# Kernel tuning notes

Measured on AMD Instinct MI355X. Metric: run time of the kernel, lower is better.

Reference implementation:

```python
import jax, jax.numpy as jnp
import numpy as np
from jax import lax


def squash(vec):
    # vec: [..., caps, dim]; squash along last dim (dim=2 in original layout [B, caps, dim])
    lensq = jnp.sum(vec * vec, axis=2)
    length = jnp.sqrt(lensq)
    scale = (lensq / (1.0 + lensq) / length)[:, :, None]
    return vec * scale


def setup_inputs() -> dict:
    key = jax.random.key(0)
    ks = jax.random.split(key, 6)
    stdv = 1.0 / np.sqrt(1152.0)
    return {
        "x": jax.random.normal(ks[0], (512, 1, 28, 28), dtype=jnp.float32),
        "conv1_w": jax.random.normal(ks[1], (256, 1, 9, 9), dtype=jnp.float32) * 0.05,
        "conv1_b": jax.random.normal(ks[2], (256,), dtype=jnp.float32) * 0.01,
        "conv2_w": jax.random.normal(ks[3], (256, 256, 9, 9), dtype=jnp.float32) * 0.01,
        "conv2_b": jax.random.normal(ks[4], (256,), dtype=jnp.float32) * 0.01,
        "caps_w": jax.random.uniform(ks[5], (1152, 8, 160), dtype=jnp.float32, minval=-stdv, maxval=stdv),
        "b_prior": jnp.zeros((1152, 10), dtype=jnp.float32),
    }


def reference(x, conv1_w, conv1_b, conv2_w, conv2_b, caps_w, b_prior):
    n_iterations = 3
    output_caps, output_dim = 10, 16
    dn = ("NCHW", "OIHW", "NCHW")

    # conv1 + relu: [N,1,28,28] -> [N,256,20,20]
    h = lax.conv_general_dilated(x, conv1_w, (1, 1), "VALID", dimension_numbers=dn)
    h = jax.nn.relu(h + conv1_b[None, :, None, None])

    # first capsule layer: conv k=9 s=2 -> [N,256,6,6]
    h = lax.conv_general_dilated(h, conv2_w, (2, 2), "VALID", dimension_numbers=dn)
    h = h + conv2_b[None, :, None, None]
    N, C, H, W = h.shape
    # [N, 32, 8, H, W] -> [N, 32, H, W, 8] -> [N, 32*H*W, 8]
    u = h.reshape(N, 32, 8, H, W).transpose(0, 1, 3, 4, 2).reshape(N, 32 * H * W, 8)
    u = squash(u)  # [N, 1152, 8]

    # prediction vectors: u_hat [N, 1152, 10, 16]
    u_hat = jnp.einsum("bid,ido->bio", u, caps_w).reshape(N, 1152, output_caps, output_dim)

    # dynamic routing-by-agreement
    c = jax.nn.softmax(b_prior, axis=1)  # [1152, 10]
    s = jnp.sum(c[None, :, :, None] * u_hat, axis=1)  # [N, 10, 16]
    v = squash(s)
    b_batch = jnp.broadcast_to(b_prior, (N, 1152, output_caps))
    for _ in range(n_iterations):
        b_batch = b_batch + jnp.sum(u_hat * v[:, None, :, :], axis=-1)  # agreement
        c = jax.nn.softmax(b_batch, axis=2)[..., None]  # [N, 1152, 10, 1]
        s = jnp.sum(c * u_hat, axis=1)
        v = squash(s)

    probs = jnp.sqrt(jnp.sum(v * v, axis=2))  # [N, 10]
    return (v, probs)
```

## Files before the change

kernel.cpp:

```cpp
#include <hip/hip_runtime.h>


#define N_IMG 512

typedef __attribute__((ext_vector_type(8))) short bf16x8;
typedef __attribute__((ext_vector_type(4))) float f32x4;
typedef __attribute__((ext_vector_type(4))) unsigned int u32x4;

__device__ __forceinline__ unsigned short f2bf(float v) {
  unsigned int uu = __float_as_uint(v);
  uu += 0x7FFF + ((uu >> 16) & 1);
  return (unsigned short)(uu >> 16);
}
__device__ __forceinline__ float bf2f(unsigned short h) {
  return __uint_as_float(((unsigned int)h) << 16);
}
__device__ __forceinline__ int swz(int row) {
  return (row ^ ((row >> 3) & 7)) << 4;
}

__global__ __launch_bounds__(256) void repack_b_kernel(
    const float* __restrict__ w2, unsigned short* __restrict__ bph,
    unsigned short* __restrict__ bpl) {
  __shared__ float slab[82 * 16 * 17];
  const int n = blockIdx.x, c = blockIdx.y;
  const int tid = threadIdx.x;
  for (int e = tid; e < 81 * 256; e += 256) {
    const int row = e / 81;
    const int rs = e - row * 81;
    const int co = row >> 4, ci = row & 15;
    slab[(rs * 16 + co) * 17 + ci] =
        w2[((size_t)(n * 16 + co) * 256 + c * 16 + ci) * 81 + rs];
  }
  __syncthreads();
  const int lane = tid & 63;
  const int l15 = lane & 15;
  const int lh = lane >> 5;
  const int cio8 = ((lane >> 4) & 1) * 8;
  for (int tt = tid >> 6; tt < 41; tt += 4) {
    const int rs = 2 * tt + lh;
    unsigned int hw[4], lw[4];
#pragma unroll
    for (int jp = 0; jp < 4; ++jp) {
      unsigned short h2[2], l2[2];
#pragma unroll
      for (int e = 0; e < 2; ++e) {
        const int j = jp * 2 + e;
        float v = (rs < 81) ? slab[(rs * 16 + l15) * 17 + cio8 + j] : 0.0f;
        unsigned short hh = f2bf(v);
        h2[e] = hh;
        l2[e] = f2bf(v - bf2f(hh));
      }
      hw[jp] = (unsigned int)h2[0] | ((unsigned int)h2[1] << 16);
      lw[jp] = (unsigned int)l2[0] | ((unsigned int)l2[1] << 16);
    }
    const size_t off = (((size_t)n * 656 + c * 41 + tt) * 64 + lane) * 8;
    *(u32x4*)(bph + off) = (u32x4){hw[0], hw[1], hw[2], hw[3]};
    *(u32x4*)(bpl + off) = (u32x4){lw[0], lw[1], lw[2], lw[3]};
  }
}

__global__ __launch_bounds__(160) void repack_cw_kernel(
    const float* __restrict__ cw, float* __restrict__ cwt) {
  __shared__ float t[8][160];
  const int i = blockIdx.x;
  const int od = threadIdx.x;
#pragma unroll
  for (int k = 0; k < 8; ++k) t[k][od] = cw[((size_t)i * 8 + k) * 160 + od];
  __syncthreads();
  float4 o0 = {t[0][od], t[1][od], t[2][od], t[3][od]};
  float4 o1 = {t[4][od], t[5][od], t[6][od], t[7][od]};
  float4* dst = (float4*)(cwt + ((size_t)i * 160 + od) * 8);
  dst[0] = o0;
  dst[1] = o1;
}

__global__ __launch_bounds__(512, 1) void fused_conv_kernel(
    const float* __restrict__ x, const float* __restrict__ w1,
    const float* __restrict__ b1, const unsigned short* __restrict__ bph,
    const unsigned short* __restrict__ bpl, const float* __restrict__ b2,
    float* __restrict__ u) {
  __shared__ __align__(16) char smem[114944];
  float* stg = (float*)(smem + 51712);
  float* img = (float*)(smem + 103424);
  float* w1l = (float*)(smem + 109696);
  float* b1l = (float*)(smem + 114880);
  float* mrg = (float*)smem;
  float* sq = (float*)smem;

  const int bp2 = blockIdx.x;
  const int tid = threadIdx.x;
  const int wid = tid >> 6;
  const int g = wid & 3;
  const int kpar = wid >> 2;
  const int lane = tid & 63;
  const int l15 = lane & 15;
  const int lq4 = lane >> 4;
  const int lqb = lq4 & 1;
  const int lh = lane >> 5;

  int rowb[5];
  bool okm[5];
#pragma unroll
  for (int mt = 0; mt < 5; ++mt) {
    const int m = mt * 16 + l15;
    okm[mt] = (m < 72);
    const int mm = okm[mt] ? m : 0;
    const int im = (mm >= 36) ? 1 : 0;
    const int p = mm - 36 * im;
    const int oy = p / 6, ox = p - 6 * oy;
    rowb[mt] = im * 400 + 40 * oy + 2 * ox;
  }

  for (int i = tid; i < 1568; i += 512) img[i] = x[bp2 * 1568 + i];
  if (tid < 16) {
    *(int*)(smem + (tid >> 2) * 12928 + 804 * 16 + (tid & 3) * 4) = 0;
  }

  f32x4 acc[5][4];
#pragma unroll
  for (int mt = 0; mt < 5; ++mt)
#pragma unroll
    for (int nn = 0; nn < 4; ++nn) acc[mt][nn] = (f32x4){0.f, 0.f, 0.f, 0.f};

  const char* hbase = smem + lqb * 12928;
  const char* lbase = smem + 25856 + lqb * 12928;
  const int tt0 = kpar ? 21 : 0;
  const int tt1 = kpar ? 41 : 21;

  for (int c = 0; c < 16; ++c) {
    __syncthreads();
    for (int i = tid; i < 1296; i += 512) w1l[i] = w1[c * 1296 + i];
    if (tid < 16) b1l[tid] = b1[c * 16 + tid];
    __syncthreads();

    for (int t = tid; t < 640; t += 512) {
      const int ig = t / 320;
      const int rest = t - ig * 320;
      const int ch = rest & 15;
      const int oy = rest >> 4;
      const float* ib = &img[ig * 784];
      float a[20];
      const float bv1 = b1l[ch];
#pragma unroll
      for (int ox = 0; ox < 20; ++ox) a[ox] = bv1;
#pragma unroll
      for (int r = 0; r < 9; ++r) {
        float row[28];
        const float4* rp = (const float4*)&ib[(oy + r) * 28];
#pragma unroll
        for (int q = 0; q < 7; ++q) {
          float4 v4 = rp[q];
          row[4 * q + 0] = v4.x; row[4 * q + 1] = v4.y;
          row[4 * q + 2] = v4.z; row[4 * q + 3] = v4.w;
        }
#pragma unroll
        for (int s = 0; s < 9; ++s) {
          const float wval = w1l[ch * 81 + r * 9 + s];
#pragma unroll
          for (int ox = 0; ox < 20; ++ox)
            a[ox] = fmaf(row[ox + s], wval, a[ox]);
        }
      }
      float4* dst = (float4*)&stg[(ig * 16 + ch) * 404 + oy * 20];
#pragma unroll
      for (int q = 0; q < 5; ++q) {
        float4 v4;
        v4.x = fmaxf(a[4 * q + 0], 0.0f);
        v4.y = fmaxf(a[4 * q + 1], 0.0f);
        v4.z = fmaxf(a[4 * q + 2], 0.0f);
        v4.w = fmaxf(a[4 * q + 3], 0.0f);
        dst[q] = v4;
      }
    }
    __syncthreads();

    for (int t = tid; t < 800; t += 512) {
      const int ig = t / 400;
      const int pos = t - ig * 400;
      const int ad = swz(t);
      unsigned int hw[8], lw[8];
#pragma unroll
      for (int jp = 0; jp < 8; ++jp) {
        unsigned short h2[2], l2[2];
#pragma unroll
        for (int e = 0; e < 2; ++e) {
          const float v = stg[(ig * 16 + jp * 2 + e) * 404 + pos];
          const unsigned short hh = f2bf(v);
          h2[e] = hh;
          l2[e] = f2bf(v - bf2f(hh));
        }
        hw[jp] = (unsigned int)h2[0] | ((unsigned int)h2[1] << 16);
        lw[jp] = (unsigned int)l2[0] | ((unsigned int)l2[1] << 16);
      }
      *(u32x4*)(smem + ad) = (u32x4){hw[0], hw[1], hw[2], hw[3]};
      *(u32x4*)(smem + 12928 + ad) = (u32x4){hw[4], hw[5], hw[6], hw[7]};
      *(u32x4*)(smem + 25856 + ad) = (u32x4){lw[0], lw[1], lw[2], lw[3]};
      *(u32x4*)(smem + 38784 + ad) = (u32x4){lw[4], lw[5], lw[6], lw[7]};
    }
    __syncthreads();

    const unsigned short* pb[4];
    const unsigned short* pl[4];
#pragma unroll
    for (int nn = 0; nn < 4; ++nn) {
      const size_t base =
          ((size_t)(g * 4 + nn) * 656 + c * 41 + tt0) * 512 + lane * 8;
      pb[nn] = bph + base;
      pl[nn] = bpl + base;
    }
    bf16x8 cbh[4], cbl[4];
#pragma unroll
    for (int nn = 0; nn < 4; ++nn) {
      cbh[nn] = *(const bf16x8*)(pb[nn]);
      cbl[nn] = *(const bf16x8*)(pl[nn]);
    }
#pragma unroll 1
    for (int tt = tt0; tt < tt1; ++tt) {
      const int nxt = (tt + 1 < tt1) ? (tt + 1 - tt0) : (tt - tt0);
      bf16x8 nbh[4], nbl[4];
#pragma unroll
      for (int nn = 0; nn < 4; ++nn) {
        nbh[nn] = *(const bf16x8*)(pb[nn] + (size_t)nxt * 512);
        nbl[nn] = *(const bf16x8*)(pl[nn] + (size_t)nxt * 512);
      }
      const int rs = 2 * tt + lh;
      const int r = (rs * 57) >> 9;
      const int s = rs - 9 * r;
      const int rs20 = 20 * r + s;
      const bool okrs = (rs <= 80);
      bf16x8 ah[5], al[5];
#pragma unroll
      for (int mt = 0; mt < 5; ++mt) {
        const int row = (okm[mt] && okrs) ? (rowb[mt] + rs20) : 800;
        const int ad = swz(row);
        ah[mt] = *(const bf16x8*)(hbase + ad);
        al[mt] = *(const bf16x8*)(lbase + ad);
      }
#pragma unroll
      for (int mt = 0; mt < 5; ++mt) {
#pragma unroll
        for (int nn = 0; nn < 4; ++nn) {
          acc[mt][nn] = __builtin_amdgcn_mfma_f32_16x16x32_bf16(
              al[mt], cbh[nn], acc[mt][nn], 0, 0, 0);
          acc[mt][nn] = __builtin_amdgcn_mfma_f32_16x16x32_bf16(
              ah[mt], cbl[nn], acc[mt][nn], 0, 0, 0);
          acc[mt][nn] = __builtin_amdgcn_mfma_f32_16x16x32_bf16(
              ah[mt], cbh[nn], acc[mt][nn], 0, 0, 0);
        }
      }
#pragma unroll
      for (int nn = 0; nn < 4; ++nn) {
        cbh[nn] = nbh[nn];
        cbl[nn] = nbl[nn];
      }
    }
  }

  __syncthreads();
  if (kpar == 1) {
#pragma unroll
    for (int mt = 0; mt < 5; ++mt)
#pragma unroll
      for (int nn = 0; nn < 4; ++nn)
        *(f32x4*)(mrg + ((((g * 5 + mt) * 4 + nn) * 64 + lane) << 2)) =
            acc[mt][nn];
  }
  __syncthreads();
  if (kpar == 0) {
#pragma unroll
    for (int mt = 0; mt < 5; ++mt)
#pragma unroll
      for (int nn = 0; nn < 4; ++nn)
        acc[mt][nn] +=
            *(const f32x4*)(mrg + ((((g * 5 + mt) * 4 + nn) * 64 + lane) << 2));
  }
  __syncthreads();
  if (kpar == 0) {
    float b2v[4];
#pragma unroll
    for (int nn = 0; nn < 4; ++nn) b2v[nn] = b2[(g * 4 + nn) * 16 + l15];
#pragma unroll
    for (int mt = 0; mt < 5; ++mt) {
#pragma unroll
      for (int i = 0; i < 4; ++i) {
        const int m = mt * 16 + lq4 * 4 + i;
        if (m < 72) {
          const int im = (m >= 36) ? 1 : 0;
          const int p36 = m - 36 * im;
#pragma unroll
          for (int nn = 0; nn < 4; ++nn) {
            sq[(im * 256 + (g * 4 + nn) * 16 + l15) * 36 + p36] =
                acc[mt][nn][i] + b2v[nn];
          }
        }
      }
    }
  }
  __syncthreads();

  for (int i = tid; i < 2304; i += 512) {
    const int ig = i / 1152;
    const int cap = i - ig * 1152;
    const int gg = cap / 36, yx = cap - 36 * gg;
    float vals[8];
    float lensq = 0.0f;
#pragma unroll
    for (int d = 0; d < 8; ++d) {
      vals[d] = sq[(ig * 256 + gg * 8 + d) * 36 + yx];
      lensq = fmaf(vals[d], vals[d], lensq);
    }
    const float len = sqrtf(lensq);
    const float scale = lensq / (1.0f + lensq) / len;
    float4* dst = (float4*)(u + ((size_t)(bp2 * 2 + ig) * 1152 + cap) * 8);
    float4 lo4, hi4;
    lo4.x = vals[0] * scale; lo4.y = vals[1] * scale;
    lo4.z = vals[2] * scale; lo4.w = vals[3] * scale;
    hi4.x = vals[4] * scale; hi4.y = vals[5] * scale;
    hi4.z = vals[6] * scale; hi4.w = vals[7] * scale;
    dst[0] = lo4; dst[1] = hi4;
  }
}

__global__ __launch_bounds__(256) void routing_a_kernel(
    const float* __restrict__ u, const float* __restrict__ cwt,
    const float* __restrict__ b_prior, const float* __restrict__ vsum,
    float* __restrict__ s_part, int pass) {
  __shared__ float u_l[64 * 8];
  __shared__ float uhat[64 * 160];
  __shared__ float b_l[64 * 10];
  __shared__ float c_l[64 * 10];
  __shared__ float v_l[160];

  const int b = blockIdx.x;
  const int ch = blockIdx.y;
  const int cap0 = ch * 64;
  const int tid = threadIdx.x;

  {
    const float* src = u + ((size_t)b * 1152 + cap0) * 8;
    for (int i = tid; i < 512; i += 256) u_l[i] = src[i];
  }
  if (pass > 0 && tid < 160) v_l[tid] = vsum[b * 160 + tid];
  __syncthreads();

  for (int idx = tid; idx < 64 * 160; idx += 256) {
    const int i = idx / 160, od = idx - 160 * i;
    const float4* wp =
        (const float4*)(cwt + ((size_t)(cap0 + i) * 160 + od) * 8);
    const float4 wa = wp[0], wb = wp[1];
    const float4 ua = *(const float4*)&u_l[i * 8];
    const float4 ub = *(const float4*)&u_l[i * 8 + 4];
    float a = ua.x * wa.x;
    a = fmaf(ua.y, wa.y, a); a = fmaf(ua.z, wa.z, a); a = fmaf(ua.w, wa.w, a);
    a = fmaf(ub.x, wb.x, a); a = fmaf(ub.y, wb.y, a);
    a = fmaf(ub.z, wb.z, a); a = fmaf(ub.w, wb.w, a);
    uhat[idx] = a;
  }
  __syncthreads();

  for (int idx = tid; idx < 640; idx += 256) {
    const int i = idx / 10, o = idx - 10 * i;
    float bb = b_prior[(cap0 + i) * 10 + o];
    if (pass > 0) {
      float agg = 0.0f;
#pragma unroll
      for (int d = 0; d < 16; ++d)
        agg = fmaf(uhat[i * 160 + o * 16 + d], v_l[o * 16 + d], agg);
      bb += agg;
    }
    b_l[idx] = bb;
  }
  __syncthreads();

  if (tid < 64) {
    float m = -1e30f;
#pragma unroll
    for (int o = 0; o < 10; ++o) m = fmaxf(m, b_l[tid * 10 + o]);
    float e[10], sum = 0.0f;
#pragma unroll
    for (int o = 0; o < 10; ++o) {
      e[o] = __expf(b_l[tid * 10 + o] - m);
      sum += e[o];
    }
    const float inv = 1.0f / sum;
#pragma unroll
    for (int o = 0; o < 10; ++o) c_l[tid * 10 + o] = e[o] * inv;
  }
  __syncthreads();

  if (tid < 160) {
    const int o = tid / 16;
    float a = 0.0f;
    for (int i = 0; i < 64; ++i)
      a = fmaf(c_l[i * 10 + o], uhat[i * 160 + tid], a);
    s_part[((size_t)ch * N_IMG + b) * 160 + tid] = a;
  }
}

__global__ __launch_bounds__(192) void routing_b_kernel(
    const float* __restrict__ s_part, float* __restrict__ v_out,
    float* __restrict__ probs, float* __restrict__ vsum, int mode) {
  __shared__ float s_l[160];
  __shared__ float scale_l[10];
  __shared__ float len_l[10];
  const int b = blockIdx.x;
  const int t = threadIdx.x;
  if (t < 160) {
    float a = 0.0f;
#pragma unroll
    for (int ch = 0; ch < 18; ++ch)
      a += s_part[((size_t)ch * N_IMG + b) * 160 + t];
    s_l[t] = a;
  }
  __syncthreads();
  if (t < 10) {
    float lensq = 0.0f;
#pragma unroll
    for (int d = 0; d < 16; ++d) {
      const float xv = s_l[t * 16 + d];
      lensq = fmaf(xv, xv, lensq);
    }
    const float len = sqrtf(lensq);
    scale_l[t] = lensq / (1.0f + lensq) / len;
    len_l[t] = lensq / (1.0f + lensq);
  }
  __syncthreads();
  if (t < 160) {
    const float vv = s_l[t] * scale_l[t / 16];
    v_out[b * 160 + t] = vv;
    if (mode == 0) vsum[b * 160 + t] = vv;
    else if (mode == 1) vsum[b * 160 + t] += vv;
  }
  if (t < 10) probs[b * 10 + t] = len_l[t];
}

extern "C" void kernel_launch(void* const* d_in, const int* in_sizes, int n_in,
                              void* d_out, int out_size, void* d_ws,
                              size_t ws_size, hipStream_t stream) {
  const float* x  = (const float*)d_in[0];
  const float* w1 = (const float*)d_in[1];
  const float* b1 = (const float*)d_in[2];
  const float* w2 = (const float*)d_in[3];
  const float* b2 = (const float*)d_in[4];
  const float* cw = (const float*)d_in[5];
  const float* bp = (const float*)d_in[6];

  float* out = (float*)d_out;
  float* v_out = out;
  float* probs = out + N_IMG * 160;

  unsigned short* bph = (unsigned short*)d_ws;
  unsigned short* bpl = bph + (size_t)16 * 656 * 512;
  float* u    = (float*)d_ws + 2 * 2686976;
  float* sp   = u + (size_t)N_IMG * 1152 * 8;
  float* vsum = sp + (size_t)18 * N_IMG * 160;
  float* cwt  = (float*)bph;

  repack_b_kernel<<<dim3(16, 16), 256, 0, stream>>>(w2, bph, bpl);
  fused_conv_kernel<<<256, 512, 0, stream>>>(x, w1, b1, bph, bpl, b2, u);
  repack_cw_kernel<<<1152, 160, 0, stream>>>(cw, cwt);
  for (int pass = 0; pass < 4; ++pass) {
    const int mode = (pass == 0) ? 0 : (pass < 3 ? 1 : 2);
    routing_a_kernel<<<dim3(N_IMG, 18), 256, 0, stream>>>(u, cwt, bp, vsum, sp,
                                                          pass);
    routing_b_kernel<<<N_IMG, 192, 0, stream>>>(sp, v_out, probs, vsum, mode);
  }
}
```

Measured before the change: 1.159 ms.

## Split conv1 rows, double-buffer B prefetch, pad LDS, store caps weights in fp16

Conv1 work is split into two half-row tasks per thread so 1280 tasks spread over 512 threads instead of 640, which evens out the load. The MFMA loop is unrolled by two with double-buffered B fragments, and the first loads are issued before the conv1 stage so global latency overlaps with it. LDS plane strides gain a 16-byte pad, likely to reduce bank conflicts. Capsule weights are stored as fp16, halving routing_a weight traffic at the cost of some precision in u_hat.

```diff
diff --git a/kernel.cpp b/kernel.cpp
--- a/kernel.cpp
+++ b/kernel.cpp
@@ -1,4 +1,5 @@
 #include <hip/hip_runtime.h>
+#include <hip/hip_fp16.h>
 
 
 #define N_IMG 512
@@ -61,18 +62,56 @@
 }
 
 __global__ __launch_bounds__(160) void repack_cw_kernel(
-    const float* __restrict__ cw, float* __restrict__ cwt) {
+    const float* __restrict__ cw, __half* __restrict__ cwt) {
   __shared__ float t[8][160];
   const int i = blockIdx.x;
   const int od = threadIdx.x;
 #pragma unroll
   for (int k = 0; k < 8; ++k) t[k][od] = cw[((size_t)i * 8 + k) * 160 + od];
   __syncthreads();
-  float4 o0 = {t[0][od], t[1][od], t[2][od], t[3][od]};
-  float4 o1 = {t[4][od], t[5][od], t[6][od], t[7][od]};
-  float4* dst = (float4*)(cwt + ((size_t)i * 160 + od) * 8);
-  dst[0] = o0;
-  dst[1] = o1;
+  u32x4 pack;
+#pragma unroll
+  for (int j = 0; j < 4; ++j) {
+    __half2 hv = __floats2half2_rn(t[2 * j][od], t[2 * j + 1][od]);
+    pack[j] = *(unsigned int*)&hv;
+  }
+  *(u32x4*)(cwt + ((size_t)i * 160 + od) * 8) = pack;
+}
+
+template <int H>
+__device__ __forceinline__ void conv1_half(const float* __restrict__ ib,
+                                           const float* __restrict__ w1l,
+                                           float* __restrict__ stg, int ch,
+                                           int oy, float bv1) {
+  float a[10];
+#pragma unroll
+  for (int ox = 0; ox < 10; ++ox) a[ox] = bv1;
+#pragma unroll
+  for (int r = 0; r < 9; ++r) {
+    float row[20];
+    const float4* rp = (const float4*)&ib[(oy + r) * 28 + H * 8];
+#pragma unroll
+    for (int q = 0; q < 5; ++q) {
+      float4 v4 = rp[q];
+      row[4 * q + 0] = v4.x; row[4 * q + 1] = v4.y;
+      row[4 * q + 2] = v4.z; row[4 * q + 3] = v4.w;
+    }
+#pragma unroll
+    for (int s = 0; s < 9; ++s) {
+      const float wval = w1l[ch * 81 + r * 9 + s];
+#pragma unroll
+      for (int ox = 0; ox < 10; ++ox)
+        a[ox] = fmaf(row[ox + s + 2 * H], wval, a[ox]);
+    }
+  }
+  float2* dst = (float2*)&stg[oy * 20 + H * 10];
+#pragma unroll
+  for (int q = 0; q < 5; ++q) {
+    float2 v2;
+    v2.x = fmaxf(a[2 * q + 0], 0.0f);
+    v2.y = fmaxf(a[2 * q + 1], 0.0f);
+    dst[q] = v2;
+  }
 }
 
 __global__ __launch_bounds__(512, 1) void fused_conv_kernel(
@@ -80,11 +119,11 @@
     const float* __restrict__ b1, const unsigned short* __restrict__ bph,
     const unsigned short* __restrict__ bpl, const float* __restrict__ b2,
     float* __restrict__ u) {
-  __shared__ __align__(16) char smem[114944];
-  float* stg = (float*)(smem + 51712);
-  float* img = (float*)(smem + 103424);
-  float* w1l = (float*)(smem + 109696);
-  float* b1l = (float*)(smem + 114880);
+  __shared__ __align__(16) char smem[115008];
+  float* stg = (float*)(smem + 51776);
+  float* img = (float*)(smem + 103488);
+  float* w1l = (float*)(smem + 109760);
+  float* b1l = (float*)(smem + 114944);
   float* mrg = (float*)smem;
   float* sq = (float*)smem;
 
@@ -114,7 +153,7 @@
 
   for (int i = tid; i < 1568; i += 512) img[i] = x[bp2 * 1568 + i];
   if (tid < 16) {
-    *(int*)(smem + (tid >> 2) * 12928 + 804 * 16 + (tid & 3) * 4) = 0;
+    *(int*)(smem + (tid >> 2) * 12944 + 804 * 16 + (tid & 3) * 4) = 0;
   }
 
   f32x4 acc[5][4];
@@ -123,55 +162,83 @@
 #pragma unroll
     for (int nn = 0; nn < 4; ++nn) acc[mt][nn] = (f32x4){0.f, 0.f, 0.f, 0.f};
 
-  const char* hbase = smem + lqb * 12928;
-  const char* lbase = smem + 25856 + lqb * 12928;
+  const char* hbase = smem + lqb * 12944;
+  const char* lbase = smem + 25888 + lqb * 12944;
   const int tt0 = kpar ? 21 : 0;
   const int tt1 = kpar ? 41 : 21;
-
+  const int nk = tt1 - tt0;
+
+#define MFMA_STEP(CBH, CBL, J, DOPF)                                       \
+  {                                                                        \
+    const int rs_ = 2 * (tt0 + (J)) + lh;                                  \
+    const int r_ = (rs_ * 57) >> 9;                                        \
+    const int s_ = rs_ - 9 * r_;                                           \
+    const int rs20_ = 20 * r_ + s_;                                        \
+    const bool okrs_ = (rs_ <= 80);                                        \
+    bf16x8 ah[5], al[5];                                                   \
+    _Pragma("unroll") for (int mt = 0; mt < 5; ++mt) {                     \
+      const int row_ = (okm[mt] && okrs_) ? (rowb[mt] + rs20_) : 800;      \
+      const int ad_ = swz(row_);                                           \
+      ah[mt] = *(const bf16x8*)(hbase + ad_);                              \
+      al[mt] = *(const bf16x8*)(lbase + ad_);                              \
+    }                                                                      \
+    _Pragma("unroll") for (int mt = 0; mt < 5; ++mt) {                     \
+      _Pragma("unroll") for (int nn = 0; nn < 4; ++nn) {                   \
+        acc[mt][nn] = __builtin_amdgcn_mfma_f32_16x16x32_bf16(             \
+            al[mt], CBH[nn], acc[mt][nn], 0, 0, 0);                        \
+        acc[mt][nn] = __builtin_amdgcn_mfma_f32_16x16x32_bf16(             \
+            ah[mt], CBL[nn], acc[mt][nn], 0, 0, 0);                        \
+        acc[mt][nn] = __builtin_amdgcn_mfma_f32_16x16x32_bf16(             \
+            ah[mt], CBH[nn], acc[mt][nn], 0, 0, 0);                        \
+      }                                                                    \
+    }                                                                      \
+    if ((DOPF) && (J) + 2 < nk) {                                          \
+      _Pragma("unroll") for (int nn = 0; nn < 4; ++nn) {                   \
+        CBH[nn] = *(const bf16x8*)(pb[nn] + (size_t)((J) + 2) * 512);      \
+        CBL[nn] = *(const bf16x8*)(pl[nn] + (size_t)((J) + 2) * 512);      \
+      }                                                                    \
+    }                                                                      \
+  }
+
+#pragma unroll 1
   for (int c = 0; c < 16; ++c) {
+    const unsigned short* pb[4];
+    const unsigned short* pl[4];
+#pragma unroll
+    for (int nn = 0; nn < 4; ++nn) {
+      const size_t base =
+          ((size_t)(g * 4 + nn) * 656 + c * 41 + tt0) * 512 + lane * 8;
+      pb[nn] = bph + base;
+      pl[nn] = bpl + base;
+    }
+    bf16x8 cbh0[4], cbl0[4], cbh1[4], cbl1[4];
+#pragma unroll
+    for (int nn = 0; nn < 4; ++nn) {
+      cbh0[nn] = *(const bf16x8*)(pb[nn]);
+      cbl0[nn] = *(const bf16x8*)(pl[nn]);
+      cbh1[nn] = *(const bf16x8*)(pb[nn] + 512);
+      cbl1[nn] = *(const bf16x8*)(pl[nn] + 512);
+    }
+
     __syncthreads();
     for (int i = tid; i < 1296; i += 512) w1l[i] = w1[c * 1296 + i];
     if (tid < 16) b1l[tid] = b1[c * 16 + tid];
     __syncthreads();
 
-    for (int t = tid; t < 640; t += 512) {
-      const int ig = t / 320;
-      const int rest = t - ig * 320;
-      const int ch = rest & 15;
-      const int oy = rest >> 4;
+    for (int t = tid; t < 1280; t += 512) {
+      const int half = (t >= 640) ? 1 : 0;
+      const int rest = t - half * 640;
+      const int ig = rest / 320;
+      const int r2 = rest - ig * 320;
+      const int ch = r2 & 15;
+      const int oy = r2 >> 4;
       const float* ib = &img[ig * 784];
-      float a[20];
+      float* sb = &stg[(ig * 16 + ch) * 404];
       const float bv1 = b1l[ch];
-#pragma unroll
-      for (int ox = 0; ox < 20; ++ox) a[ox] = bv1;
-#pragma unroll
-      for (int r = 0; r < 9; ++r) {
-        float row[28];
-        const float4* rp = (const float4*)&ib[(oy + r) * 28];
-#pragma unroll
-        for (int q = 0; q < 7; ++q) {
-          float4 v4 = rp[q];
-          row[4 * q + 0] = v4.x; row[4 * q + 1] = v4.y;
-          row[4 * q + 2] = v4.z; row[4 * q + 3] = v4.w;
-        }
-#pragma unroll
-        for (int s = 0; s < 9; ++s) {
-          const float wval = w1l[ch * 81 + r * 9 + s];
-#pragma unroll
-          for (int ox = 0; ox < 20; ++ox)
-            a[ox] = fmaf(row[ox + s], wval, a[ox]);
-        }
-      }
-      float4* dst = (float4*)&stg[(ig * 16 + ch) * 404 + oy * 20];
-#pragma unroll
-      for (int q = 0; q < 5; ++q) {
-        float4 v4;
-        v4.x = fmaxf(a[4 * q + 0], 0.0f);
-        v4.y = fmaxf(a[4 * q + 1], 0.0f);
-        v4.z = fmaxf(a[4 * q + 2], 0.0f);
-        v4.w = fmaxf(a[4 * q + 3], 0.0f);
-        dst[q] = v4;
-      }
+      if (half == 0)
+        conv1_half<0>(ib, w1l, sb, ch, oy, bv1);
+      else
+        conv1_half<1>(ib, w1l, sb, ch, oy, bv1);
     }
     __syncthreads();
 
@@ -194,68 +261,21 @@
         lw[jp] = (unsigned int)l2[0] | ((unsigned int)l2[1] << 16);
       }
       *(u32x4*)(smem + ad) = (u32x4){hw[0], hw[1], hw[2], hw[3]};
-      *(u32x4*)(smem + 12928 + ad) = (u32x4){hw[4], hw[5], hw[6], hw[7]};
-      *(u32x4*)(smem + 25856 + ad) = (u32x4){lw[0], lw[1], lw[2], lw[3]};
-      *(u32x4*)(smem + 38784 + ad) = (u32x4){lw[4], lw[5], lw[6], lw[7]};
+      *(u32x4*)(smem + 12944 + ad) = (u32x4){hw[4], hw[5], hw[6], hw[7]};
+      *(u32x4*)(smem + 25888 + ad) = (u32x4){lw[0], lw[1], lw[2], lw[3]};
+      *(u32x4*)(smem + 38832 + ad) = (u32x4){lw[4], lw[5], lw[6], lw[7]};
     }
     __syncthreads();
 
-    const unsigned short* pb[4];
-    const unsigned short* pl[4];
-#pragma unroll
-    for (int nn = 0; nn < 4; ++nn) {
-      const size_t base =
-          ((size_t)(g * 4 + nn) * 656 + c * 41 + tt0) * 512 + lane * 8;
-      pb[nn] = bph + base;
-      pl[nn] = bpl + base;
-    }
-    bf16x8 cbh[4], cbl[4];
-#pragma unroll
-    for (int nn = 0; nn < 4; ++nn) {
-      cbh[nn] = *(const bf16x8*)(pb[nn]);
-      cbl[nn] = *(const bf16x8*)(pl[nn]);
-    }
+    int j = 0;
 #pragma unroll 1
-    for (int tt = tt0; tt < tt1; ++tt) {
-      const int nxt = (tt + 1 < tt1) ? (tt + 1 - tt0) : (tt - tt0);
-      bf16x8 nbh[4], nbl[4];
-#pragma unroll
-      for (int nn = 0; nn < 4; ++nn) {
-        nbh[nn] = *(const bf16x8*)(pb[nn] + (size_t)nxt * 512);
-        nbl[nn] = *(const bf16x8*)(pl[nn] + (size_t)nxt * 512);
-      }
-      const int rs = 2 * tt + lh;
-      const int r = (rs * 57) >> 9;
-      const int s = rs - 9 * r;
-      const int rs20 = 20 * r + s;
-      const bool okrs = (rs <= 80);
-      bf16x8 ah[5], al[5];
-#pragma unroll
-      for (int mt = 0; mt < 5; ++mt) {
-        const int row = (okm[mt] && okrs) ? (rowb[mt] + rs20) : 800;
-        const int ad = swz(row);
-        ah[mt] = *(const bf16x8*)(hbase + ad);
-        al[mt] = *(const bf16x8*)(lbase + ad);
-      }
-#pragma unroll
-      for (int mt = 0; mt < 5; ++mt) {
-#pragma unroll
-        for (int nn = 0; nn < 4; ++nn) {
-          acc[mt][nn] = __builtin_amdgcn_mfma_f32_16x16x32_bf16(
-              al[mt], cbh[nn], acc[mt][nn], 0, 0, 0);
-          acc[mt][nn] = __builtin_amdgcn_mfma_f32_16x16x32_bf16(
-              ah[mt], cbl[nn], acc[mt][nn], 0, 0, 0);
-          acc[mt][nn] = __builtin_amdgcn_mfma_f32_16x16x32_bf16(
-              ah[mt], cbh[nn], acc[mt][nn], 0, 0, 0);
-        }
-      }
-#pragma unroll
-      for (int nn = 0; nn < 4; ++nn) {
-        cbh[nn] = nbh[nn];
-        cbl[nn] = nbl[nn];
-      }
-    }
-  }
+    for (; j + 1 < nk; j += 2) {
+      MFMA_STEP(cbh0, cbl0, j, 1);
+      MFMA_STEP(cbh1, cbl1, j + 1, 1);
+    }
+    if (j < nk) MFMA_STEP(cbh0, cbl0, j, 0);
+  }
+#undef MFMA_STEP
 
   __syncthreads();
   if (kpar == 1) {
@@ -323,7 +343,7 @@
 }
 
 __global__ __launch_bounds__(256) void routing_a_kernel(
-    const float* __restrict__ u, const float* __restrict__ cwt,
+    const float* __restrict__ u, const __half* __restrict__ cwt,
     const float* __restrict__ b_prior, const float* __restrict__ vsum,
     float* __restrict__ s_part, int pass) {
   __shared__ float u_l[64 * 8];
@@ -346,15 +366,26 @@
 
   for (int idx = tid; idx < 64 * 160; idx += 256) {
     const int i = idx / 160, od = idx - 160 * i;
-    const float4* wp =
-        (const float4*)(cwt + ((size_t)(cap0 + i) * 160 + od) * 8);
-    const float4 wa = wp[0], wb = wp[1];
+    const u32x4 wv = *(const u32x4*)(cwt + ((size_t)(cap0 + i) * 160 + od) * 8);
     const float4 ua = *(const float4*)&u_l[i * 8];
     const float4 ub = *(const float4*)&u_l[i * 8 + 4];
-    float a = ua.x * wa.x;
-    a = fmaf(ua.y, wa.y, a); a = fmaf(ua.z, wa.z, a); a = fmaf(ua.w, wa.w, a);
-    a = fmaf(ub.x, wb.x, a); a = fmaf(ub.y, wb.y, a);
-    a = fmaf(ub.z, wb.z, a); a = fmaf(ub.w, wb.w, a);
+    __half2 h0, h1, h2, h3;
+    *(unsigned int*)&h0 = wv[0];
+    *(unsigned int*)&h1 = wv[1];
+    *(unsigned int*)&h2 = wv[2];
+    *(unsigned int*)&h3 = wv[3];
+    const float2 f0 = __half22float2(h0);
+    const float2 f1 = __half22float2(h1);
+    const float2 f2 = __half22float2(h2);
+    const float2 f3 = __half22float2(h3);
+    float a = ua.x * f0.x;
+    a = fmaf(ua.y, f0.y, a);
+    a = fmaf(ua.z, f1.x, a);
+    a = fmaf(ua.w, f1.y, a);
+    a = fmaf(ub.x, f2.x, a);
+    a = fmaf(ub.y, f2.y, a);
+    a = fmaf(ub.z, f3.x, a);
+    a = fmaf(ub.w, f3.y, a);
     uhat[idx] = a;
   }
   __syncthreads();
@@ -455,15 +486,15 @@
   float* u    = (float*)d_ws + 2 * 2686976;
   float* sp   = u + (size_t)N_IMG * 1152 * 8;
   float* vsum = sp + (size_t)18 * N_IMG * 160;
-  float* cwt  = (float*)bph;
+  __half* cwth = (__half*)bph;
 
   repack_b_kernel<<<dim3(16, 16), 256, 0, stream>>>(w2, bph, bpl);
   fused_conv_kernel<<<256, 512, 0, stream>>>(x, w1, b1, bph, bpl, b2, u);
-  repack_cw_kernel<<<1152, 160, 0, stream>>>(cw, cwt);
+  repack_cw_kernel<<<1152, 160, 0, stream>>>(cw, cwth);
   for (int pass = 0; pass < 4; ++pass) {
     const int mode = (pass == 0) ? 0 : (pass < 3 ? 1 : 2);
-    routing_a_kernel<<<dim3(N_IMG, 18), 256, 0, stream>>>(u, cwt, bp, vsum, sp,
-                                                          pass);
+    routing_a_kernel<<<dim3(N_IMG, 18), 256, 0, stream>>>(u, cwth, bp, vsum,
+                                                          sp, pass);
     routing_b_kernel<<<N_IMG, 192, 0, stream>>>(sp, v_out, probs, vsum, mode);
   }
 }
```

Result: slower. 1.290 ms (+11.3%).
